# Kernel optimization log

Measured on AMD Instinct MI355X. Metric: run time of the kernel, lower is better.

Reference implementation:

```python
import jax, jax.numpy as jnp
import numpy as np

GAMMA = 1.0  # gamma=1, train_gamma=False -> constant
K = 3        # kernel_size


def _l2norm(x, axis=-1):
    return x / jnp.sqrt(jnp.sum(x * x, axis=axis, keepdims=True))


def setup_inputs() -> dict:
    key = jax.random.key(0)
    ks = jax.random.split(key, 9)
    B_img, R, D = 48, 36, 1024
    B_cap, T = 48, 32
    Dq = D // 4  # reduce_proj = 4
    s = lambda fan: 1.0 / np.sqrt(fan)
    return {
        "img_embed": jax.random.normal(ks[0], (B_img, R, D), jnp.float32),
        "cap_embed": jax.random.normal(ks[1], (B_cap, T, D), jnp.float32),
        "lens": jax.random.randint(ks[2], (B_cap,), 1, T),
        "Wred": jax.random.normal(ks[3], (Dq, D), jnp.float32) * s(D),
        "bred": jax.random.normal(ks[4], (Dq,), jnp.float32) * s(D),
        "Wproj": jax.random.normal(ks[5], (D * K, Dq), jnp.float32) * s(Dq),
        "bproj": jax.random.normal(ks[6], (D * K,), jnp.float32) * s(Dq),
        "Wconv": jax.random.normal(ks[7], (D, D), jnp.float32) * s(D),
        "bconv": jax.random.normal(ks[8], (D,), jnp.float32) * s(D),
    }


def reference(img_embed, cap_embed, lens, Wred, bred, Wproj, bproj, Wconv, bconv):
    # img_embed: (B, R, D) -> x: (B, D, R);  cap_embed: (Q, T, D)
    B, R, D = img_embed.shape
    Q = cap_embed.shape[0]
    x = jnp.transpose(img_embed, (0, 2, 1))  # (B, D, R)

    # red_txt Conv1d(D, D/4, 1): only token 0 is used downstream
    cap0 = cap_embed[:, 0, :]                                 # (Q, D)
    cap_repr = cap0 @ Wred.T + bred                           # (Q, D/4)

    # dynamic depthwise kernel, softmax-normalized over the K taps
    wdyn = (cap_repr @ Wproj.T + bproj).reshape(Q, D, K)      # (Q, D, K)
    wdyn = jax.nn.softmax(wdyn, axis=-1)

    # depthwise conv (padding=1) applied to the FULL image batch per caption
    xpad = jnp.pad(x, ((0, 0), (0, 0), (1, 1)))
    shifts = jnp.stack([xpad[:, :, h:h + R] for h in range(K)], axis=-1)  # (B,D,R,K)
    conv_dyn = jnp.einsum('bcrk,qck->qbcr', shifts, wdyn)      # (Q, B, D, R)

    # pointwise Conv1d(D, D, 1)
    y = jnp.einsum('qbcr,dc->qbdr', conv_dyn, Wconv) + bconv[None, None, :, None]

    # softmax gate over regions, gated sum-pool, l2norm, cosine sim
    mask = jax.nn.softmax(y * GAMMA, axis=-1)
    img_vec = _l2norm(jnp.sum(mask * y, axis=-1), axis=-1)     # (Q, B, D)
    cap_vec = _l2norm(cap0, axis=-1)                           # (Q, D)
    sims = jnp.einsum('qbd,qd->bq', img_vec, cap_vec)          # (B_img, B_cap)
    return sims
```

## Files before the change

kernel.cpp:

```cpp
#include <hip/hip_runtime.h>

#define D_   1024
#define B_   48
#define Q_   48
#define R_   36
#define RP_  38
#define DQ_  256
#define NPQ_ 1728

typedef __attribute__((ext_vector_type(8))) short bf16x8;
typedef __attribute__((ext_vector_type(8))) unsigned short u16x8;
typedef __attribute__((ext_vector_type(4))) float f32x4;

static __device__ __forceinline__ unsigned short f2bf(float f) {
  union { float f; unsigned u; } v; v.f = f;
  unsigned r = v.u + 0x7fffu + ((v.u >> 16) & 1u);
  return (unsigned short)(r >> 16);
}
static __device__ __forceinline__ float bf2f(unsigned short h) {
  union { unsigned u; float f; } v; v.u = ((unsigned)h) << 16; return v.f;
}
static __device__ __forceinline__ void gload_lds16(const void* g, void* s) {
  __builtin_amdgcn_global_load_lds(
      (const __attribute__((address_space(1))) unsigned int*)g,
      (__attribute__((address_space(3))) unsigned int*)s, 16, 0, 0);
}

__global__ __launch_bounds__(256) void k_pre(
    const float* __restrict__ img, unsigned short* __restrict__ xpb,
    const float* __restrict__ Wconv, unsigned short* __restrict__ wcbf,
    const float* __restrict__ cap_embed, const float* __restrict__ Wred,
    const float* __restrict__ bred, float* __restrict__ repr)
{
  const int bx = blockIdx.x, t = threadIdx.x;
  if (bx < B_ * RP_) {
    const int b = bx / RP_, rp = bx % RP_;
    const int c = t * 4;
    short4 o;
    if (rp == 0 || rp == RP_ - 1) { o.x = 0; o.y = 0; o.z = 0; o.w = 0; }
    else {
      float4 v = *(const float4*)&img[((size_t)b * R_ + (rp-1)) * D_ + c];
      o.x = (short)f2bf(v.x); o.y = (short)f2bf(v.y);
      o.z = (short)f2bf(v.z); o.w = (short)f2bf(v.w);
    }
    *(short4*)&xpb[(size_t)bx * D_ + c] = o;
  } else if (bx < B_ * RP_ + 512) {
    const int tid = (bx - B_ * RP_) * 256 + t;
    const int m = tid >> 7;
    const int gg = tid & 127;
    const int tile = gg >> 2, g = gg & 3;
    const int gl = g ^ ((m >> 1) & 3);
    const float* src = Wconv + (size_t)m * D_ + tile * 32 + gl * 8;
    float4 v0 = *(const float4*)src, v1 = *(const float4*)(src + 4);
    u16x8 o;
    o[0] = f2bf(v0.x); o[1] = f2bf(v0.y); o[2] = f2bf(v0.z); o[3] = f2bf(v0.w);
    o[4] = f2bf(v1.x); o[5] = f2bf(v1.y); o[6] = f2bf(v1.z); o[7] = f2bf(v1.w);
    *(u16x8*)&wcbf[(size_t)m * D_ + tile * 32 + g * 8] = o;
  } else {
    const int b2 = bx - (B_ * RP_ + 512);
    const int q = b2 >> 6, yo = b2 & 63;
    const int w = t >> 6, lane = t & 63;
    const int o = yo * 4 + w;
    const float4* c4 = (const float4*)(cap_embed + (size_t)q * 32 * D_);
    const float4* wr = (const float4*)(Wred + (size_t)o * D_);
    float acc = 0.f;
    #pragma unroll
    for (int j = 0; j < 4; j++) {
      float4 a = wr[lane + j*64], c = c4[lane + j*64];
      acc += a.x*c.x + a.y*c.y + a.z*c.z + a.w*c.w;
    }
    #pragma unroll
    for (int off = 32; off > 0; off >>= 1) acc += __shfl_down(acc, off);
    if (lane == 0) repr[(size_t)q * DQ_ + o] = acc + bred[o];
  }
}

__global__ __launch_bounds__(256) void k_wdyn(const float* __restrict__ repr,
    const float* __restrict__ Wproj, const float* __restrict__ bproj,
    float* __restrict__ wpl)
{
  const int q = blockIdx.x;
  const int w = threadIdx.x >> 6, lane = threadIdx.x & 63;
  const int d = blockIdx.y * 4 + w;
  float4 r4 = ((const float4*)(repr + (size_t)q * DQ_))[lane];
  float a0, a1, a2;
  {
    const float4* p0 = (const float4*)(Wproj + (size_t)(d*3 + 0) * DQ_);
    const float4* p1 = (const float4*)(Wproj + (size_t)(d*3 + 1) * DQ_);
    const float4* p2 = (const float4*)(Wproj + (size_t)(d*3 + 2) * DQ_);
    float4 v0 = p0[lane], v1 = p1[lane], v2 = p2[lane];
    a0 = v0.x*r4.x + v0.y*r4.y + v0.z*r4.z + v0.w*r4.w;
    a1 = v1.x*r4.x + v1.y*r4.y + v1.z*r4.z + v1.w*r4.w;
    a2 = v2.x*r4.x + v2.y*r4.y + v2.z*r4.z + v2.w*r4.w;
  }
  #pragma unroll
  for (int off = 32; off > 0; off >>= 1) {
    a0 += __shfl_down(a0, off);
    a1 += __shfl_down(a1, off);
    a2 += __shfl_down(a2, off);
  }
  if (lane == 0) {
    float l0 = a0 + bproj[d*3], l1 = a1 + bproj[d*3+1], l2 = a2 + bproj[d*3+2];
    float m = fmaxf(l0, fmaxf(l1, l2));
    float e0 = __expf(l0-m), e1 = __expf(l1-m), e2 = __expf(l2-m);
    float inv = 1.0f / (e0 + e1 + e2);
    wpl[((size_t)q*3 + 0) * D_ + d] = e0 * inv;
    wpl[((size_t)q*3 + 1) * D_ + d] = e1 * inv;
    wpl[((size_t)q*3 + 2) * D_ + d] = e2 * inv;
  }
}

__global__ __launch_bounds__(256) void k_cd(const unsigned short* __restrict__ xpb,
    const float* __restrict__ wpl, unsigned short* __restrict__ cd, int qstart)
{
  const int ql = blockIdx.y, qg = qstart + ql;
  const int t = threadIdx.x;
  const int bloc = t >> 7;
  const int b = blockIdx.x * 2 + bloc;
  const int gg = t & 127;
  const int tile = gg >> 2, g = gg & 3;
  const int ch = gg * 8;

  float w0[8], w1[8], w2[8];
  {
    const float4* p0 = (const float4*)(wpl + ((size_t)qg*3 + 0)*D_ + ch);
    const float4* p1 = (const float4*)(wpl + ((size_t)qg*3 + 1)*D_ + ch);
    const float4* p2 = (const float4*)(wpl + ((size_t)qg*3 + 2)*D_ + ch);
    float4 a0 = p0[0], a1 = p0[1], b0 = p1[0], b1 = p1[1], d0 = p2[0], d1 = p2[1];
    w0[0]=a0.x; w0[1]=a0.y; w0[2]=a0.z; w0[3]=a0.w; w0[4]=a1.x; w0[5]=a1.y; w0[6]=a1.z; w0[7]=a1.w;
    w1[0]=b0.x; w1[1]=b0.y; w1[2]=b0.z; w1[3]=b0.w; w1[4]=b1.x; w1[5]=b1.y; w1[6]=b1.z; w1[7]=b1.w;
    w2[0]=d0.x; w2[1]=d0.y; w2[2]=d0.z; w2[3]=d0.w; w2[4]=d1.x; w2[5]=d1.y; w2[6]=d1.z; w2[7]=d1.w;
  }
  const unsigned short* xb = xpb + (size_t)b * RP_ * D_ + ch;
  u16x8 ra = *(const u16x8*)&xb[0];
  u16x8 rb = *(const u16x8*)&xb[D_];
  unsigned short* outb = cd + ((size_t)ql * NPQ_ + (size_t)b * R_) * D_ + tile * 32;
  for (int r = 0; r < R_; r++) {
    u16x8 rc = *(const u16x8*)&xb[(size_t)(r + 2) * D_];
    u16x8 o;
    #pragma unroll
    for (int i = 0; i < 8; i++) {
      float y = w0[i]*bf2f(ra[i]) + w1[i]*bf2f(rb[i]) + w2[i]*bf2f(rc[i]);
      o[i] = f2bf(y);
    }
    int gp = g ^ (((b * 36 + r) >> 1) & 3);
    *(u16x8*)&outb[(size_t)r * D_ + gp * 8] = o;
    ra = rb; rb = rc;
  }
}

#define BM_ 256
#define BN_ 144
#define BK_ 64

__global__ __launch_bounds__(256, 2) void k_gemm(
    const unsigned short* __restrict__ wcbf, const unsigned short* __restrict__ cd,
    const float* __restrict__ bconv, float* __restrict__ imgvec, int qstart)
{
  __shared__ __align__(16) unsigned char smem[51200];
  unsigned short* As = (unsigned short*)smem;
  unsigned short* Bs = (unsigned short*)(smem + 32768);
  float* ep = (float*)smem;

  const int t = threadIdx.x;
  const int w = t >> 6, lane = t & 63;
  const int nt0 = blockIdx.x * BN_;
  const int dt0 = blockIdx.y * BM_;
  const int ql = blockIdx.z, qg = qstart + ql;

  f32x4 acc[4][9];
  #pragma unroll
  for (int mm = 0; mm < 4; mm++)
    #pragma unroll
    for (int nt = 0; nt < 9; nt++)
      acc[mm][nt] = (f32x4){0.f, 0.f, 0.f, 0.f};

  const int lrow = lane >> 2;
  const int lc8  = (lane & 3) * 8;
  const unsigned short* Ag = wcbf + (size_t)dt0 * D_ + lc8;
  const unsigned short* Bg = cd + ((size_t)ql * NPQ_ + nt0) * D_ + lc8;
  const int fr = lane & 15;
  const int fro = fr * 32 + ((((lane >> 4) ^ ((fr >> 1) & 3))) << 3);

  for (int k0 = 0; k0 < D_; k0 += BK_) {
    #pragma unroll
    for (int jj = 0; jj < 8; jj++) {
      int u = w + jj * 4;
      int ja = u >> 1, h = u & 1;
      gload_lds16(Ag + (size_t)(ja*16 + lrow) * D_ + k0 + h*32, As + u * 512);
    }
    for (int u = w; u < 18; u += 4) {
      int jb = u >> 1, h = u & 1;
      gload_lds16(Bg + (size_t)(jb*16 + lrow) * D_ + k0 + h*32, Bs + u * 512);
    }
    __syncthreads();
    #pragma unroll
    for (int s = 0; s < 2; s++) {
      bf16x8 aF[4], bF[9];
      #pragma unroll
      for (int mm = 0; mm < 4; mm++)
        aF[mm] = *(const bf16x8*)&As[((w*4 + mm)*2 + s) * 512 + fro];
      #pragma unroll
      for (int nt = 0; nt < 9; nt++)
        bF[nt] = *(const bf16x8*)&Bs[(nt*2 + s) * 512 + fro];
      #pragma unroll
      for (int mm = 0; mm < 4; mm++)
        #pragma unroll
        for (int nt = 0; nt < 9; nt++)
          acc[mm][nt] = __builtin_amdgcn_mfma_f32_16x16x32_bf16(aF[mm], bF[nt], acc[mm][nt], 0, 0, 0);
    }
    __syncthreads();
  }

  const int quad = lane >> 4;
  const int b0 = nt0 / R_;
  #pragma unroll
  for (int pp = 0; pp < 2; pp++) {
    #pragma unroll
    for (int p = 0; p < 2; p++) {
      if ((w >> 1) == pp) {
        #pragma unroll
        for (int mm = 0; mm < 4; mm++)
          #pragma unroll
          for (int nt = 0; nt < 9; nt++) {
            int col = nt * 16 + fr;
            int cl = col - 72 * p;
            if (cl >= 0 && cl < 72) {
              #pragma unroll
              for (int rg = 0; rg < 4; rg++) {
                int rloc = (w & 1) * 64 + mm * 16 + quad * 4 + rg;
                ep[rloc * 73 + cl] = acc[mm][nt][rg];
              }
            }
          }
      }
      __syncthreads();
      {
        int dloc = t >> 1, bloc = t & 1;
        int bg = b0 + p * 2 + bloc;
        int dg = dt0 + pp * 128 + dloc;
        const float* yr = ep + dloc * 73 + bloc * 36;
        float m = yr[0];
        for (int r = 1; r < R_; r++) m = fmaxf(m, yr[r]);
        float s = 0.f, wsum = 0.f;
        for (int r = 0; r < R_; r++) {
          float yv = yr[r];
          float e = __expf(yv - m);
          s += e; wsum += e * yv;
        }
        float img = wsum / s + bconv[dg];
        imgvec[((size_t)qg * B_ + bg) * D_ + dg] = img;
      }
      __syncthreads();
    }
  }
}

__global__ __launch_bounds__(256) void k_sims(const float* __restrict__ imgvec,
    const float* __restrict__ cap_embed, float* __restrict__ out)
{
  const int q = blockIdx.x, b = blockIdx.y, t = threadIdx.x;
  const float4* iv = (const float4*)(imgvec + ((size_t)q * B_ + b) * D_);
  const float4* cv = (const float4*)(cap_embed + (size_t)q * 32 * D_);
  float4 a = iv[t], c = cv[t];
  float ss = a.x*a.x + a.y*a.y + a.z*a.z + a.w*a.w;
  float sc = c.x*c.x + c.y*c.y + c.z*c.z + c.w*c.w;
  float dt = a.x*c.x + a.y*c.y + a.z*c.z + a.w*c.w;
  #pragma unroll
  for (int off = 32; off > 0; off >>= 1) {
    ss += __shfl_down(ss, off);
    sc += __shfl_down(sc, off);
    dt += __shfl_down(dt, off);
  }
  __shared__ float r1[4], r2[4], r3[4];
  if ((t & 63) == 0) { r1[t >> 6] = ss; r2[t >> 6] = sc; r3[t >> 6] = dt; }
  __syncthreads();
  if (t == 0) {
    ss = r1[0] + r1[1] + r1[2] + r1[3];
    sc = r2[0] + r2[1] + r2[2] + r2[3];
    dt = r3[0] + r3[1] + r3[2] + r3[3];
    out[(size_t)b * Q_ + q] = dt * rsqrtf(ss) * rsqrtf(sc);
  }
}

extern "C" void kernel_launch(void* const* d_in, const int* in_sizes, int n_in,
                              void* d_out, int out_size, void* d_ws, size_t ws_size,
                              hipStream_t stream)
{
  (void)in_sizes; (void)n_in; (void)out_size;
  const float* img   = (const float*)d_in[0];
  const float* cap   = (const float*)d_in[1];
  const float* Wred  = (const float*)d_in[3];
  const float* bred  = (const float*)d_in[4];
  const float* Wproj = (const float*)d_in[5];
  const float* bproj = (const float*)d_in[6];
  const float* Wconv = (const float*)d_in[7];
  const float* bconv = (const float*)d_in[8];
  float* out = (float*)d_out;

  char* ws = (char*)d_ws;
  const size_t XPB_B  = (size_t)B_ * RP_ * D_ * 2;
  const size_t WCBF_B = (size_t)D_ * D_ * 2;
  const size_t WPL_B  = (size_t)Q_ * 3 * D_ * 4;
  const size_t REPR_B = (size_t)Q_ * DQ_ * 4;
  const size_t IMGV_B = (size_t)Q_ * B_ * D_ * 4;
  unsigned short* xpb  = (unsigned short*)ws;
  unsigned short* wcbf = (unsigned short*)(ws + XPB_B);
  float* wpl    = (float*)(ws + XPB_B + WCBF_B);
  float* repr   = (float*)(ws + XPB_B + WCBF_B + WPL_B);
  float* imgvec = (float*)(ws + XPB_B + WCBF_B + WPL_B + REPR_B);
  const size_t FIXED = XPB_B + WCBF_B + WPL_B + REPR_B + IMGV_B;
  unsigned short* cdbuf = (unsigned short*)(ws + FIXED);
  const size_t PERQ = (size_t)NPQ_ * D_ * 2;

  int qchunk = 1;
  if (ws_size > FIXED + PERQ) {
    size_t c = (ws_size - FIXED) / PERQ;
    qchunk = (c > (size_t)Q_) ? Q_ : (int)c;
  }

  k_pre<<<dim3(B_ * RP_ + 512 + Q_ * 64), dim3(256), 0, stream>>>(
      img, xpb, Wconv, wcbf, cap, Wred, bred, repr);
  k_wdyn<<<dim3(Q_, 256), dim3(256), 0, stream>>>(repr, Wproj, bproj, wpl);
  for (int q0 = 0; q0 < Q_; q0 += qchunk) {
    int qs = (Q_ - q0 < qchunk) ? (Q_ - q0) : qchunk;
    k_cd<<<dim3(B_ / 2, qs), dim3(256), 0, stream>>>(xpb, wpl, cdbuf, q0);
    k_gemm<<<dim3(NPQ_ / BN_, D_ / BM_, qs), dim3(256), 0, stream>>>(wcbf, cdbuf, bconv, imgvec, q0);
  }
  k_sims<<<dim3(Q_, B_), dim3(256), 0, stream>>>(imgvec, cap, out);
}
```

Baseline: 288.7 us.

## Fuse l2norm and cosine reductions into GEMM epilogue with atomics

The GEMM epilogue now accumulates per-(q,b) partial sums of img·img and img·cap directly and atomically adds them into a small buffer, instead of writing the full Q×B×D imgvec tensor. The separate sims kernel is replaced by a tiny finalize kernel, and caption norms are computed in the pre-kernel. This removes the large imgvec write and read-back plus one full pass. In exchange it adds a memset, float atomics with nondeterministic summation order, and a little extra epilogue work.

```diff
diff --git a/kernel.cpp b/kernel.cpp
--- a/kernel.cpp
+++ b/kernel.cpp
@@ -30,9 +30,11 @@
     const float* __restrict__ img, unsigned short* __restrict__ xpb,
     const float* __restrict__ Wconv, unsigned short* __restrict__ wcbf,
     const float* __restrict__ cap_embed, const float* __restrict__ Wred,
-    const float* __restrict__ bred, float* __restrict__ repr)
+    const float* __restrict__ bred, float* __restrict__ repr,
+    float* __restrict__ scq)
 {
   const int bx = blockIdx.x, t = threadIdx.x;
+  __shared__ float red[4];
   if (bx < B_ * RP_) {
     const int b = bx / RP_, rp = bx % RP_;
     const int c = t * 4;
@@ -56,7 +58,7 @@
     o[0] = f2bf(v0.x); o[1] = f2bf(v0.y); o[2] = f2bf(v0.z); o[3] = f2bf(v0.w);
     o[4] = f2bf(v1.x); o[5] = f2bf(v1.y); o[6] = f2bf(v1.z); o[7] = f2bf(v1.w);
     *(u16x8*)&wcbf[(size_t)m * D_ + tile * 32 + g * 8] = o;
-  } else {
+  } else if (bx < B_ * RP_ + 512 + Q_ * 64) {
     const int b2 = bx - (B_ * RP_ + 512);
     const int q = b2 >> 6, yo = b2 & 63;
     const int w = t >> 6, lane = t & 63;
@@ -72,6 +74,16 @@
     #pragma unroll
     for (int off = 32; off > 0; off >>= 1) acc += __shfl_down(acc, off);
     if (lane == 0) repr[(size_t)q * DQ_ + o] = acc + bred[o];
+  } else {
+    const int q = bx - (B_ * RP_ + 512 + Q_ * 64);
+    const int w = t >> 6, lane = t & 63;
+    float4 v = ((const float4*)(cap_embed + (size_t)q * 32 * D_))[t];
+    float ss = v.x*v.x + v.y*v.y + v.z*v.z + v.w*v.w;
+    #pragma unroll
+    for (int off = 32; off > 0; off >>= 1) ss += __shfl_down(ss, off);
+    if (lane == 0) red[w] = ss;
+    __syncthreads();
+    if (t == 0) scq[q] = red[0] + red[1] + red[2] + red[3];
   }
 }
 
@@ -155,7 +167,8 @@
 
 __global__ __launch_bounds__(256, 2) void k_gemm(
     const unsigned short* __restrict__ wcbf, const unsigned short* __restrict__ cd,
-    const float* __restrict__ bconv, float* __restrict__ imgvec, int qstart)
+    const float* __restrict__ bconv, const float* __restrict__ cap_embed,
+    float* __restrict__ accbuf, int qstart)
 {
   __shared__ __align__(16) unsigned char smem[51200];
   unsigned short* As = (unsigned short*)smem;
@@ -214,8 +227,12 @@
 
   const int quad = lane >> 4;
   const int b0 = nt0 / R_;
+  float pss[2] = {0.f, 0.f}, pdt[2] = {0.f, 0.f};
   #pragma unroll
   for (int pp = 0; pp < 2; pp++) {
+    const int dg = dt0 + pp * 128 + (t >> 1);
+    const float capv = cap_embed[(size_t)qg * 32 * D_ + dg];
+    const float bcv = bconv[dg];
     #pragma unroll
     for (int p = 0; p < 2; p++) {
       if ((w >> 1) == pp) {
@@ -236,10 +253,7 @@
       }
       __syncthreads();
       {
-        int dloc = t >> 1, bloc = t & 1;
-        int bg = b0 + p * 2 + bloc;
-        int dg = dt0 + pp * 128 + dloc;
-        const float* yr = ep + dloc * 73 + bloc * 36;
+        const float* yr = ep + (t >> 1) * 73 + (t & 1) * 36;
         float m = yr[0];
         for (int r = 1; r < R_; r++) m = fmaxf(m, yr[r]);
         float s = 0.f, wsum = 0.f;
@@ -248,39 +262,37 @@
           float e = __expf(yv - m);
           s += e; wsum += e * yv;
         }
-        float img = wsum / s + bconv[dg];
-        imgvec[((size_t)qg * B_ + bg) * D_ + dg] = img;
+        float img = wsum / s + bcv;
+        pss[p] += img * img;
+        pdt[p] += img * capv;
       }
       __syncthreads();
     }
   }
-}
-
-__global__ __launch_bounds__(256) void k_sims(const float* __restrict__ imgvec,
-    const float* __restrict__ cap_embed, float* __restrict__ out)
-{
-  const int q = blockIdx.x, b = blockIdx.y, t = threadIdx.x;
-  const float4* iv = (const float4*)(imgvec + ((size_t)q * B_ + b) * D_);
-  const float4* cv = (const float4*)(cap_embed + (size_t)q * 32 * D_);
-  float4 a = iv[t], c = cv[t];
-  float ss = a.x*a.x + a.y*a.y + a.z*a.z + a.w*a.w;
-  float sc = c.x*c.x + c.y*c.y + c.z*c.z + c.w*c.w;
-  float dt = a.x*c.x + a.y*c.y + a.z*c.z + a.w*c.w;
   #pragma unroll
-  for (int off = 32; off > 0; off >>= 1) {
-    ss += __shfl_down(ss, off);
-    sc += __shfl_down(sc, off);
-    dt += __shfl_down(dt, off);
-  }
-  __shared__ float r1[4], r2[4], r3[4];
-  if ((t & 63) == 0) { r1[t >> 6] = ss; r2[t >> 6] = sc; r3[t >> 6] = dt; }
-  __syncthreads();
-  if (t == 0) {
-    ss = r1[0] + r1[1] + r1[2] + r1[3];
-    sc = r2[0] + r2[1] + r2[2] + r2[3];
-    dt = r3[0] + r3[1] + r3[2] + r3[3];
-    out[(size_t)b * Q_ + q] = dt * rsqrtf(ss) * rsqrtf(sc);
-  }
+  for (int p = 0; p < 2; p++) {
+    float ssv = pss[p], dtv = pdt[p];
+    #pragma unroll
+    for (int off = 32; off >= 2; off >>= 1) {
+      ssv += __shfl_down(ssv, off);
+      dtv += __shfl_down(dtv, off);
+    }
+    if (lane < 2) {
+      int bg = b0 + p * 2 + lane;
+      atomicAdd(&accbuf[((size_t)qg * B_ + bg) * 2 + 0], ssv);
+      atomicAdd(&accbuf[((size_t)qg * B_ + bg) * 2 + 1], dtv);
+    }
+  }
+}
+
+__global__ __launch_bounds__(256) void k_fin(const float* __restrict__ accbuf,
+    const float* __restrict__ scq, float* __restrict__ out)
+{
+  const int id = blockIdx.x * 256 + threadIdx.x;
+  const int b = id / Q_, q = id % Q_;
+  float ss = accbuf[((size_t)q * B_ + b) * 2 + 0];
+  float dt = accbuf[((size_t)q * B_ + b) * 2 + 1];
+  out[id] = dt * rsqrtf(ss) * rsqrtf(scq[q]);
 }
 
 extern "C" void kernel_launch(void* const* d_in, const int* in_sizes, int n_in,
@@ -303,13 +315,15 @@
   const size_t WCBF_B = (size_t)D_ * D_ * 2;
   const size_t WPL_B  = (size_t)Q_ * 3 * D_ * 4;
   const size_t REPR_B = (size_t)Q_ * DQ_ * 4;
-  const size_t IMGV_B = (size_t)Q_ * B_ * D_ * 4;
+  const size_t ACC_B  = (size_t)Q_ * B_ * 2 * 4;
+  const size_t SCQ_B  = 256 * 4;
   unsigned short* xpb  = (unsigned short*)ws;
   unsigned short* wcbf = (unsigned short*)(ws + XPB_B);
   float* wpl    = (float*)(ws + XPB_B + WCBF_B);
   float* repr   = (float*)(ws + XPB_B + WCBF_B + WPL_B);
-  float* imgvec = (float*)(ws + XPB_B + WCBF_B + WPL_B + REPR_B);
-  const size_t FIXED = XPB_B + WCBF_B + WPL_B + REPR_B + IMGV_B;
+  float* accbuf = (float*)(ws + XPB_B + WCBF_B + WPL_B + REPR_B);
+  float* scq    = (float*)(ws + XPB_B + WCBF_B + WPL_B + REPR_B + ACC_B);
+  const size_t FIXED = XPB_B + WCBF_B + WPL_B + REPR_B + ACC_B + SCQ_B;
   unsigned short* cdbuf = (unsigned short*)(ws + FIXED);
   const size_t PERQ = (size_t)NPQ_ * D_ * 2;
 
@@ -319,13 +333,15 @@
     qchunk = (c > (size_t)Q_) ? Q_ : (int)c;
   }
 
-  k_pre<<<dim3(B_ * RP_ + 512 + Q_ * 64), dim3(256), 0, stream>>>(
-      img, xpb, Wconv, wcbf, cap, Wred, bred, repr);
+  hipMemsetAsync(accbuf, 0, ACC_B, stream);
+  k_pre<<<dim3(B_ * RP_ + 512 + Q_ * 64 + Q_), dim3(256), 0, stream>>>(
+      img, xpb, Wconv, wcbf, cap, Wred, bred, repr, scq);
   k_wdyn<<<dim3(Q_, 256), dim3(256), 0, stream>>>(repr, Wproj, bproj, wpl);
   for (int q0 = 0; q0 < Q_; q0 += qchunk) {
     int qs = (Q_ - q0 < qchunk) ? (Q_ - q0) : qchunk;
     k_cd<<<dim3(B_ / 2, qs), dim3(256), 0, stream>>>(xpb, wpl, cdbuf, q0);
-    k_gemm<<<dim3(NPQ_ / BN_, D_ / BM_, qs), dim3(256), 0, stream>>>(wcbf, cdbuf, bconv, imgvec, q0);
-  }
-  k_sims<<<dim3(Q_, B_), dim3(256), 0, stream>>>(imgvec, cap, out);
-}
+    k_gemm<<<dim3(NPQ_ / BN_, D_ / BM_, qs), dim3(256), 0, stream>>>(
+        wcbf, cdbuf, bconv, cap, accbuf, q0);
+  }
+  k_fin<<<dim3((Q_ * B_) / 256), dim3(256), 0, stream>>>(accbuf, scq, out);
+}
```

After: 373.1 us. +29.3%, slower.
